# Performance work log

Hardware: AMD Instinct MI355X
Metric: run time of the kernel (lower is better)

## Reference

```python
import jax, jax.numpy as jnp
import numpy as np

B = 4096
D_IN = 4096
N_REC = 4096
TAU = 20.0
THR = 1.0
DT = 1.0
N_REF = 5
DAMP = 0.3
DECAY = float(np.exp(-DT / TAU))


def spike_function(v_scaled):
    # Heaviside step; gradient (used only in fwdbwd module) is the pseudo-derivative.
    return (v_scaled > 0.0).astype(jnp.float32)


def setup_inputs() -> dict:
    key = jax.random.key(0)
    k1, k2, k3, k4, k5, k6 = jax.random.split(key, 6)
    inputs = jax.random.normal(k1, (B, D_IN), jnp.float32)
    v0 = jax.random.normal(k2, (B, N_REC), jnp.float32) * 0.5
    r0 = jax.random.randint(k3, (B, N_REC), 0, N_REF + 1, jnp.int32)
    z0 = (jax.random.uniform(k4, (B, N_REC)) < 0.1).astype(jnp.float32)  # binary spikes
    # GlorotNormal: std = sqrt(2 / (fan_in + fan_out))
    w_in = (jax.random.normal(k5, (D_IN, N_REC), jnp.float32)
            * np.sqrt(2.0 / (D_IN + N_REC)).astype(np.float32))
    w_rec = (jax.random.normal(k6, (N_REC, N_REC), jnp.float32)
             * np.sqrt(2.0 / (N_REC + N_REC)).astype(np.float32))
    return {"inputs": inputs, "v0": v0, "r0": r0, "z0": z0, "w_in": w_in, "w_rec": w_rec}


def reference(inputs, v0, r0, z0, w_in, w_rec):
    # Zero self-connections (diagonal disconnect mask)
    eye = jnp.eye(N_REC, dtype=w_rec.dtype)
    w_rec_nd = w_rec * (1.0 - eye)

    i_in = inputs @ w_in                    # [B, N_REC]
    i_rec = z0 @ w_rec_nd                   # [B, N_REC]
    i_reset = -THR * z0
    input_current = (1.0 - DECAY) * (i_in + i_rec) + i_reset
    new_v = DECAY * v0 + input_current

    v_scaled = (new_v - THR) / THR
    new_z = spike_function(v_scaled)
    new_z = jnp.where(r0 > 0, 0.0, new_z)   # refractory masking
    new_r = jnp.clip(r0 - 1 + (new_z * N_REF).astype(jnp.int32), 0, N_REF)
    return (new_v, new_z, new_r)
```

## Files before the change

kernel.cpp:

```cpp
#include <hip/hip_runtime.h>
#include <cstdint>
#include <cstddef>


typedef __attribute__((ext_vector_type(8))) _Float16 f16x8;
typedef __attribute__((ext_vector_type(4))) float f32x4;

#define DECAY_F 0.9512294245007140f
#define ONEMD_F 0.0487705754992860f

#define BAR() __builtin_amdgcn_s_barrier()
#define WAITV(n) asm volatile("s_waitcnt vmcnt(" #n ")" ::: "memory")

__device__ __forceinline__ void gl2lds16(const void* g, void* s) {
  __builtin_amdgcn_global_load_lds(
      (const __attribute__((address_space(1))) uint32_t*)g,
      (__attribute__((address_space(3))) uint32_t*)s, 16, 0, 0);
}

__global__ __launch_bounds__(256) void prep_all(const float* __restrict__ w_in,
                                                const float* __restrict__ w_rec,
                                                const float* __restrict__ inputs,
                                                const float* __restrict__ z0,
                                                _Float16* __restrict__ wtH,
                                                _Float16* __restrict__ wtL,
                                                _Float16* __restrict__ aH,
                                                _Float16* __restrict__ aL) {
  int bid = blockIdx.x;
  int t = threadIdx.x;
  if (bid < 8192) {
    __shared__ float s[64][65];
    int kt = bid >> 6, nt = bid & 63;
    int k0 = kt * 64, n0 = nt * 64;

    bool rec = (k0 >= 4096);
    const float* W = rec ? w_rec : w_in;
    int kb = rec ? (k0 - 4096) : k0;

    int cr = t >> 4;
    int cc = (t & 15) * 4;
#pragma unroll
    for (int j = 0; j < 4; ++j) {
      int r = cr + j * 16;
      float4 v = *reinterpret_cast<const float4*>(&W[(size_t)(kb + r) * 4096 + n0 + cc]);
      s[r][cc + 0] = v.x; s[r][cc + 1] = v.y; s[r][cc + 2] = v.z; s[r][cc + 3] = v.w;
    }
    __syncthreads();
#pragma unroll
    for (int j = 0; j < 2; ++j) {
      int g = t + 256 * j;
      int n = g >> 3;
      int k8 = (g & 7) * 8;
      f16x8 h, l;
#pragma unroll
      for (int i = 0; i < 8; ++i) {
        float w = s[k8 + i][n];
        int gk = k0 + k8 + i;
        if (rec && (gk - 4096) == (n0 + n)) w = 0.0f;
        w *= 256.0f;
        _Float16 hi = (_Float16)w;
        h[i] = hi;
        l[i] = (_Float16)(w - (float)hi);
      }
      size_t o = (size_t)(n0 + n) * 8192 + (size_t)(k0 + k8);
      *reinterpret_cast<f16x8*>(&wtH[o]) = h;
      *reinterpret_cast<f16x8*>(&wtL[o]) = l;
    }
  } else {
    int g = (bid - 8192) * 256 + t;
    int b = g >> 9;
    int k8 = (g & 511) * 8;

    const float4* pi = reinterpret_cast<const float4*>(&inputs[(size_t)b * 4096 + k8]);
    float4 x = pi[0], y = pi[1];
    float xs[8] = {x.x, x.y, x.z, x.w, y.x, y.y, y.z, y.w};
    f16x8 h, l;
#pragma unroll
    for (int i = 0; i < 8; ++i) {
      _Float16 hi = (_Float16)xs[i];
      h[i] = hi;
      l[i] = (_Float16)(xs[i] - (float)hi);
    }
    *reinterpret_cast<f16x8*>(&aH[(size_t)b * 8192 + k8]) = h;
    *reinterpret_cast<f16x8*>(&aL[(size_t)b * 4096 + k8]) = l;

    const float4* pz = reinterpret_cast<const float4*>(&z0[(size_t)b * 4096 + k8]);
    x = pz[0]; y = pz[1];
    float zs[8] = {x.x, x.y, x.z, x.w, y.x, y.y, y.z, y.w};
    f16x8 hz;
#pragma unroll
    for (int i = 0; i < 8; ++i) hz[i] = (_Float16)zs[i];
    *reinterpret_cast<f16x8*>(&aH[(size_t)b * 8192 + 4096 + k8]) = hz;
  }
}

#define DO_MFMA(AF, BF, MH, NH)                                              \
  __builtin_amdgcn_s_setprio(1);                                             \
  _Pragma("unroll")                                                          \
  for (int j_ = 0; j_ < 4; ++j_)                                             \
    _Pragma("unroll")                                                        \
    for (int i_ = 0; i_ < 2; ++i_)                                           \
      _Pragma("unroll")                                                      \
      for (int kh_ = 0; kh_ < 2; ++kh_)                                      \
        acc[MH][j_][NH][i_] = __builtin_amdgcn_mfma_f32_16x16x32_f16(        \
            AF[j_][kh_], BF[i_][kh_], acc[MH][j_][NH][i_], 0, 0, 0);         \
  __builtin_amdgcn_s_setprio(0);

template <int FUSED>
__global__ __launch_bounds__(512, 2) void lif_gemm(const _Float16* __restrict__ aH,
                                                   const _Float16* __restrict__ aL,
                                                   const _Float16* __restrict__ wtH,
                                                   const _Float16* __restrict__ wtL,
                                                   const float* __restrict__ v0,
                                                   const int* __restrict__ r0,
                                                   const float* __restrict__ z0,
                                                   float* __restrict__ o0,
                                                   float* __restrict__ o1,
                                                   float* __restrict__ o2) {
  extern __shared__ __align__(16) char lds[];

  int bid = blockIdx.x;
  int swz = (bid & 7) * 32 + (bid >> 3);
  int bm = swz >> 4, bn = swz & 15;
  int row0 = bm << 8, col0 = bn << 8;

  int t = threadIdx.x;
  int w = t >> 6, lane = t & 63;
  int wm = w >> 2, wn = w & 3;
  int wm16 = wm << 4, wn16 = wn << 4;
  int rl = lane & 15, klane = lane >> 4;
  int lr = lane >> 3;
  int sg = (lane & 7) ^ lr;

  f32x4 acc[2][4][2][2];
#pragma unroll
  for (int a = 0; a < 2; ++a)
#pragma unroll
    for (int b = 0; b < 4; ++b)
#pragma unroll
      for (int c = 0; c < 2; ++c)
#pragma unroll
        for (int d = 0; d < 2; ++d) acc[a][b][c][d] = (f32x4){0.f, 0.f, 0.f, 0.f};

  auto stageA = [&](int buf, int half, const _Float16* A, int strA, int kb) {
#pragma unroll
    for (int c = 0; c < 2; ++c) {
      int gr = row0 + (half << 7) + (w << 4) + (c << 3) + lr;
      const char* src = (const char*)A + (((size_t)gr * strA + kb) << 1) + (sg << 4);
      char* dst = lds + (buf << 16) + (half << 14) + ((w * 2 + c) << 10);
      gl2lds16(src, dst);
    }
  };
  auto stageB = [&](int buf, int half, const _Float16* Bp, int kb) {
#pragma unroll
    for (int c = 0; c < 2; ++c) {
      int gc = col0 + (half << 7) + (w << 4) + (c << 3) + lr;
      const char* src = (const char*)Bp + (((size_t)gc * 8192 + kb) << 1) + (sg << 4);
      char* dst = lds + (buf << 16) + 32768 + (half << 14) + ((w * 2 + c) << 10);
      gl2lds16(src, dst);
    }
  };
  auto ldsFragA = [&](int buf, int half, int j, int kh) -> f16x8 {
    int r = (j << 5) + wm16 + rl;
    int kb = (kh << 6) + (klane << 4);
    int byte = (buf << 16) + (half << 14) + (r << 7) + (kb ^ ((r & 7) << 4));
    return *(const f16x8*)(lds + byte);
  };
  auto ldsFragB = [&](int buf, int half, int i, int kh) -> f16x8 {
    int r = (i << 6) + wn16 + rl;
    int kb = (kh << 6) + (klane << 4);
    int byte = (buf << 16) + 32768 + (half << 14) + (r << 7) + (kb ^ ((r & 7) << 4));
    return *(const f16x8*)(lds + byte);
  };
  auto segOf = [&](int tt, const _Float16*& A, const _Float16*& Bp, int& kb, int& strA) {
    if (tt < 128)      { A = aH; Bp = wtH; kb = tt << 6;         strA = 8192; }
    else if (tt < 256) { A = aH; Bp = wtL; kb = (tt - 128) << 6; strA = 8192; }
    else               { A = aL; Bp = wtH; kb = (tt - 256) << 6; strA = 4096; }
  };

  {
    const _Float16 *A, *Bp; int kb, strA;
    segOf(0, A, Bp, kb, strA);
    stageA(0, 0, A, strA, kb);
    stageA(0, 1, A, strA, kb);
    stageB(0, 0, Bp, kb);
    stageB(0, 1, Bp, kb);
  }
  WAITV(2);
  BAR();

  f16x8 a0f[4][2], a1f[4][2], b0f[2][2], b1f[2][2];

  for (int tau = 0; tau < 320; ++tau) {
    int cur = tau & 1, nxt = cur ^ 1;
    int nt = tau + 1;
    bool hn = nt < 320;
    const _Float16 *An = aH, *Bn = wtH; int kbn = 0, strAn = 8192;
    if (hn) segOf(nt, An, Bn, kbn, strAn);

#pragma unroll
    for (int j = 0; j < 4; ++j)
#pragma unroll
      for (int kh = 0; kh < 2; ++kh) a0f[j][kh] = ldsFragA(cur, 0, j, kh);
#pragma unroll
    for (int i = 0; i < 2; ++i)
#pragma unroll
      for (int kh = 0; kh < 2; ++kh) b0f[i][kh] = ldsFragB(cur, 0, i, kh);
    if (hn) stageA(nxt, 0, An, strAn, kbn);
    DO_MFMA(a0f, b0f, 0, 0);

#pragma unroll
    for (int j = 0; j < 4; ++j)
#pragma unroll
      for (int kh = 0; kh < 2; ++kh) a1f[j][kh] = ldsFragA(cur, 1, j, kh);
    if (hn) stageA(nxt, 1, An, strAn, kbn);
    DO_MFMA(a1f, b0f, 1, 0);
    if (tau == 319) { WAITV(0); } else { WAITV(4); }
    BAR();

#pragma unroll
    for (int i = 0; i < 2; ++i)
#pragma unroll
      for (int kh = 0; kh < 2; ++kh) b1f[i][kh] = ldsFragB(cur, 1, i, kh);
    if (hn) stageB(nxt, 0, Bn, kbn);
    DO_MFMA(a0f, b1f, 0, 1);

    if (hn) stageB(nxt, 1, Bn, kbn);
    DO_MFMA(a1f, b1f, 1, 1);
    if (hn) { WAITV(2); }
    BAR();
  }

  const float invW = 1.0f / 256.0f;
#pragma unroll
  for (int mh = 0; mh < 2; ++mh)
#pragma unroll
    for (int j = 0; j < 4; ++j)
#pragma unroll
      for (int nh = 0; nh < 2; ++nh)
#pragma unroll
        for (int i = 0; i < 2; ++i) {
          int row = row0 + (mh << 7) + (j << 5) + wm16 + (klane << 2);
          int col = col0 + (nh << 7) + (i << 6) + wn16 + rl;
#pragma unroll
          for (int jj = 0; jj < 4; ++jj) {
            size_t idx = (size_t)(row + jj) * 4096 + col;
            float S = acc[mh][j][nh][i][jj] * invW;
            if (FUSED) {
              float nv = DECAY_F * v0[idx] + (ONEMD_F * S - z0[idx]);
              bool spike = (nv > 1.0f) && (r0[idx] <= 0);
              int nr = r0[idx] - 1 + (spike ? 5 : 0);
              nr = nr < 0 ? 0 : (nr > 5 ? 5 : nr);
              o0[idx] = nv;
              o1[idx] = spike ? 1.0f : 0.0f;
              o2[idx] = (float)nr;
            } else {
              o0[idx] = S;
            }
          }
        }
}

__global__ __launch_bounds__(256) void lif_epilogue(const float* __restrict__ v0,
                                                    const int* __restrict__ r0,
                                                    const float* __restrict__ z0,
                                                    float* __restrict__ outv,
                                                    float* __restrict__ outz,
                                                    float* __restrict__ outr) {
  size_t i = ((size_t)blockIdx.x * 256 + threadIdx.x) * 4;
  float4 S = *reinterpret_cast<const float4*>(&outv[i]);
  float4 V = *reinterpret_cast<const float4*>(&v0[i]);
  float4 Z = *reinterpret_cast<const float4*>(&z0[i]);
  int4 R = *reinterpret_cast<const int4*>(&r0[i]);
  float s[4] = {S.x, S.y, S.z, S.w};
  float v[4] = {V.x, V.y, V.z, V.w};
  float z[4] = {Z.x, Z.y, Z.z, Z.w};
  int r[4] = {R.x, R.y, R.z, R.w};
  float4 ov, oz, orr;
  float* po[3] = {&ov.x, &oz.x, &orr.x};
#pragma unroll
  for (int j = 0; j < 4; ++j) {
    float nv = DECAY_F * v[j] + (ONEMD_F * s[j] - z[j]);
    bool spike = (nv > 1.0f) && (r[j] <= 0);
    int nr = r[j] - 1 + (spike ? 5 : 0);
    nr = nr < 0 ? 0 : (nr > 5 ? 5 : nr);
    po[0][j] = nv;
    po[1][j] = spike ? 1.0f : 0.0f;
    po[2][j] = (float)nr;
  }
  *reinterpret_cast<float4*>(&outv[i]) = ov;
  *reinterpret_cast<float4*>(&outz[i]) = oz;
  *reinterpret_cast<float4*>(&outr[i]) = orr;
}

extern "C" void kernel_launch(void* const* d_in, const int* in_sizes, int n_in,
                              void* d_out, int out_size, void* d_ws, size_t ws_size,
                              hipStream_t stream) {
  const float* inputs = (const float*)d_in[0];
  const float* v0     = (const float*)d_in[1];
  const int*   r0     = (const int*)d_in[2];
  const float* z0     = (const float*)d_in[3];
  const float* w_in   = (const float*)d_in[4];
  const float* w_rec  = (const float*)d_in[5];

  const size_t MB = (size_t)1 << 20;
  if (ws_size < 128 * MB) return;
  bool fused = (ws_size >= 224 * MB);

  _Float16* wtH = (_Float16*)d_ws;
  _Float16* wtL = (_Float16*)((char*)d_ws + 64 * MB);

  float* out  = (float*)d_out;
  float* outv = out;
  float* outz = out + (size_t)4096 * 4096;
  float* outr = out + (size_t)2 * 4096 * 4096;

  _Float16* aH;
  _Float16* aL;
  if (fused) {
    aH = (_Float16*)((char*)d_ws + 128 * MB);
    aL = (_Float16*)((char*)d_ws + 192 * MB);
  } else {
    aH = (_Float16*)outz;
    aL = (_Float16*)outr;
  }

  (void)hipFuncSetAttribute((const void*)lif_gemm<1>,
                            hipFuncAttributeMaxDynamicSharedMemorySize, 131072);
  (void)hipFuncSetAttribute((const void*)lif_gemm<0>,
                            hipFuncAttributeMaxDynamicSharedMemorySize, 131072);

  prep_all<<<dim3(16384), dim3(256), 0, stream>>>(w_in, w_rec, inputs, z0,
                                                  wtH, wtL, aH, aL);
  if (fused) {
    lif_gemm<1><<<dim3(256), dim3(512), 131072, stream>>>(
        aH, aL, wtH, wtL, v0, r0, z0, outv, outz, outr);
  } else {
    lif_gemm<0><<<dim3(256), dim3(512), 131072, stream>>>(
        aH, aL, wtH, wtL, v0, r0, z0, outv, outz, outr);
    lif_epilogue<<<dim3(16384), dim3(256), 0, stream>>>(v0, r0, z0, outv, outz, outr);
  }
}
```

Baseline: 662.4 us.

## Double waves per GEMM block to 16 and stream A fragments per phase

Raises the GEMM block from 8 to 16 waves, so each wave owns a 32x32 sub-tile per quadrant instead of 64x32. This halves the per-wave accumulators and loads A fragments from LDS just before their MFMAs rather than holding them all in registers. The global-to-LDS staging is redistributed to one load per wave, and the wait counts are adjusted to match. The aim is more waves in flight to hide latency, at the cost of more LDS fragment reads per MFMA and possible LDS bandwidth pressure. The launch bound of 1024 threads with 4 blocks cannot be met given 128KB of LDS per block.

```diff
diff --git a/kernel.cpp b/kernel.cpp
--- a/kernel.cpp
+++ b/kernel.cpp
@@ -94,29 +94,32 @@
   }
 }
 
-#define DO_MFMA(AF, BF, MH, NH)                                              \
-  __builtin_amdgcn_s_setprio(1);                                             \
+#define MFMA_(A_, B_, C_) __builtin_amdgcn_mfma_f32_16x16x32_f16(A_, B_, C_, 0, 0, 0)
+
+#define PHASE(BUF, MH, NH, BF)                                               \
   _Pragma("unroll")                                                          \
-  for (int j_ = 0; j_ < 4; ++j_)                                             \
-    _Pragma("unroll")                                                        \
-    for (int i_ = 0; i_ < 2; ++i_)                                           \
-      _Pragma("unroll")                                                      \
-      for (int kh_ = 0; kh_ < 2; ++kh_)                                      \
-        acc[MH][j_][NH][i_] = __builtin_amdgcn_mfma_f32_16x16x32_f16(        \
-            AF[j_][kh_], BF[i_][kh_], acc[MH][j_][NH][i_], 0, 0, 0);         \
-  __builtin_amdgcn_s_setprio(0);
+  for (int kh_ = 0; kh_ < 2; ++kh_) {                                        \
+    f16x8 a0_ = ldsFragA(BUF, MH, 0, kh_);                                   \
+    f16x8 a1_ = ldsFragA(BUF, MH, 1, kh_);                                   \
+    __builtin_amdgcn_s_setprio(1);                                           \
+    acc[MH][0][NH][0] = MFMA_(a0_, BF[0][kh_], acc[MH][0][NH][0]);           \
+    acc[MH][0][NH][1] = MFMA_(a0_, BF[1][kh_], acc[MH][0][NH][1]);           \
+    acc[MH][1][NH][0] = MFMA_(a1_, BF[0][kh_], acc[MH][1][NH][0]);           \
+    acc[MH][1][NH][1] = MFMA_(a1_, BF[1][kh_], acc[MH][1][NH][1]);           \
+    __builtin_amdgcn_s_setprio(0);                                           \
+  }
 
 template <int FUSED>
-__global__ __launch_bounds__(512, 2) void lif_gemm(const _Float16* __restrict__ aH,
-                                                   const _Float16* __restrict__ aL,
-                                                   const _Float16* __restrict__ wtH,
-                                                   const _Float16* __restrict__ wtL,
-                                                   const float* __restrict__ v0,
-                                                   const int* __restrict__ r0,
-                                                   const float* __restrict__ z0,
-                                                   float* __restrict__ o0,
-                                                   float* __restrict__ o1,
-                                                   float* __restrict__ o2) {
+__global__ __launch_bounds__(1024, 4) void lif_gemm(const _Float16* __restrict__ aH,
+                                                    const _Float16* __restrict__ aL,
+                                                    const _Float16* __restrict__ wtH,
+                                                    const _Float16* __restrict__ wtL,
+                                                    const float* __restrict__ v0,
+                                                    const int* __restrict__ r0,
+                                                    const float* __restrict__ z0,
+                                                    float* __restrict__ o0,
+                                                    float* __restrict__ o1,
+                                                    float* __restrict__ o2) {
   extern __shared__ __align__(16) char lds[];
 
   int bid = blockIdx.x;
@@ -127,47 +130,40 @@
   int t = threadIdx.x;
   int w = t >> 6, lane = t & 63;
   int wm = w >> 2, wn = w & 3;
-  int wm16 = wm << 4, wn16 = wn << 4;
   int rl = lane & 15, klane = lane >> 4;
   int lr = lane >> 3;
   int sg = (lane & 7) ^ lr;
 
-  f32x4 acc[2][4][2][2];
+  f32x4 acc[2][2][2][2];
 #pragma unroll
   for (int a = 0; a < 2; ++a)
 #pragma unroll
-    for (int b = 0; b < 4; ++b)
+    for (int b = 0; b < 2; ++b)
 #pragma unroll
       for (int c = 0; c < 2; ++c)
 #pragma unroll
         for (int d = 0; d < 2; ++d) acc[a][b][c][d] = (f32x4){0.f, 0.f, 0.f, 0.f};
 
   auto stageA = [&](int buf, int half, const _Float16* A, int strA, int kb) {
-#pragma unroll
-    for (int c = 0; c < 2; ++c) {
-      int gr = row0 + (half << 7) + (w << 4) + (c << 3) + lr;
-      const char* src = (const char*)A + (((size_t)gr * strA + kb) << 1) + (sg << 4);
-      char* dst = lds + (buf << 16) + (half << 14) + ((w * 2 + c) << 10);
-      gl2lds16(src, dst);
-    }
+    int gr = row0 + (half << 7) + (w << 3) + lr;
+    const char* src = (const char*)A + (((size_t)gr * strA + kb) << 1) + (sg << 4);
+    char* dst = lds + (buf << 16) + (half << 14) + (w << 10);
+    gl2lds16(src, dst);
   };
   auto stageB = [&](int buf, int half, const _Float16* Bp, int kb) {
-#pragma unroll
-    for (int c = 0; c < 2; ++c) {
-      int gc = col0 + (half << 7) + (w << 4) + (c << 3) + lr;
-      const char* src = (const char*)Bp + (((size_t)gc * 8192 + kb) << 1) + (sg << 4);
-      char* dst = lds + (buf << 16) + 32768 + (half << 14) + ((w * 2 + c) << 10);
-      gl2lds16(src, dst);
-    }
+    int gc = col0 + (half << 7) + (w << 3) + lr;
+    const char* src = (const char*)Bp + (((size_t)gc * 8192 + kb) << 1) + (sg << 4);
+    char* dst = lds + (buf << 16) + 32768 + (half << 14) + (w << 10);
+    gl2lds16(src, dst);
   };
   auto ldsFragA = [&](int buf, int half, int j, int kh) -> f16x8 {
-    int r = (j << 5) + wm16 + rl;
+    int r = (wm << 5) + (j << 4) + rl;
     int kb = (kh << 6) + (klane << 4);
     int byte = (buf << 16) + (half << 14) + (r << 7) + (kb ^ ((r & 7) << 4));
     return *(const f16x8*)(lds + byte);
   };
   auto ldsFragB = [&](int buf, int half, int i, int kh) -> f16x8 {
-    int r = (i << 6) + wn16 + rl;
+    int r = (wn << 5) + (i << 4) + rl;
     int kb = (kh << 6) + (klane << 4);
     int byte = (buf << 16) + 32768 + (half << 14) + (r << 7) + (kb ^ ((r & 7) << 4));
     return *(const f16x8*)(lds + byte);
@@ -186,10 +182,10 @@
     stageB(0, 0, Bp, kb);
     stageB(0, 1, Bp, kb);
   }
-  WAITV(2);
+  WAITV(1);
   BAR();
 
-  f16x8 a0f[4][2], a1f[4][2], b0f[2][2], b1f[2][2];
+  f16x8 b0f[2][2], b1f[2][2];
 
   for (int tau = 0; tau < 320; ++tau) {
     int cur = tau & 1, nxt = cur ^ 1;
@@ -199,23 +195,15 @@
     if (hn) segOf(nt, An, Bn, kbn, strAn);
 
 #pragma unroll
-    for (int j = 0; j < 4; ++j)
-#pragma unroll
-      for (int kh = 0; kh < 2; ++kh) a0f[j][kh] = ldsFragA(cur, 0, j, kh);
-#pragma unroll
     for (int i = 0; i < 2; ++i)
 #pragma unroll
       for (int kh = 0; kh < 2; ++kh) b0f[i][kh] = ldsFragB(cur, 0, i, kh);
     if (hn) stageA(nxt, 0, An, strAn, kbn);
-    DO_MFMA(a0f, b0f, 0, 0);
-
-#pragma unroll
-    for (int j = 0; j < 4; ++j)
-#pragma unroll
-      for (int kh = 0; kh < 2; ++kh) a1f[j][kh] = ldsFragA(cur, 1, j, kh);
+    PHASE(cur, 0, 0, b0f);
+
     if (hn) stageA(nxt, 1, An, strAn, kbn);
-    DO_MFMA(a1f, b0f, 1, 0);
-    if (tau == 319) { WAITV(0); } else { WAITV(4); }
+    PHASE(cur, 1, 0, b0f);
+    if (tau == 319) { WAITV(0); } else { WAITV(2); }
     BAR();
 
 #pragma unroll
@@ -223,11 +211,11 @@
 #pragma unroll
       for (int kh = 0; kh < 2; ++kh) b1f[i][kh] = ldsFragB(cur, 1, i, kh);
     if (hn) stageB(nxt, 0, Bn, kbn);
-    DO_MFMA(a0f, b1f, 0, 1);
+    PHASE(cur, 0, 1, b1f);
 
     if (hn) stageB(nxt, 1, Bn, kbn);
-    DO_MFMA(a1f, b1f, 1, 1);
-    if (hn) { WAITV(2); }
+    PHASE(cur, 1, 1, b1f);
+    if (hn) { WAITV(1); }
     BAR();
   }
 
@@ -235,13 +223,13 @@
 #pragma unroll
   for (int mh = 0; mh < 2; ++mh)
 #pragma unroll
-    for (int j = 0; j < 4; ++j)
+    for (int j = 0; j < 2; ++j)
 #pragma unroll
       for (int nh = 0; nh < 2; ++nh)
 #pragma unroll
         for (int i = 0; i < 2; ++i) {
-          int row = row0 + (mh << 7) + (j << 5) + wm16 + (klane << 2);
-          int col = col0 + (nh << 7) + (i << 6) + wn16 + rl;
+          int row = row0 + (mh << 7) + (wm << 5) + (j << 4) + (klane << 2);
+          int col = col0 + (nh << 7) + (wn << 5) + (i << 4) + rl;
 #pragma unroll
           for (int jj = 0; jj < 4; ++jj) {
             size_t idx = (size_t)(row + jj) * 4096 + col;
@@ -333,10 +321,10 @@
   prep_all<<<dim3(16384), dim3(256), 0, stream>>>(w_in, w_rec, inputs, z0,
                                                   wtH, wtL, aH, aL);
   if (fused) {
-    lif_gemm<1><<<dim3(256), dim3(512), 131072, stream>>>(
+    lif_gemm<1><<<dim3(256), dim3(1024), 131072, stream>>>(
         aH, aL, wtH, wtL, v0, r0, z0, outv, outz, outr);
   } else {
-    lif_gemm<0><<<dim3(256), dim3(512), 131072, stream>>>(
+    lif_gemm<0><<<dim3(256), dim3(1024), 131072, stream>>>(
         aH, aL, wtH, wtL, v0, r0, z0, outv, outz, outr);
     lif_epilogue<<<dim3(16384), dim3(256), 0, stream>>>(v0, r0, z0, outv, outz, outr);
   }
```

Measured after the change: 719.4 us. 1.09x slower.
